# Kernel tuning notes

Hardware: AMD Instinct MI355X
Metric: run time of the kernel (lower is better)

Reference implementation:

```python
import jax, jax.numpy as jnp
import numpy as np

N, E, IN, ED, OUT = 50000, 800000, 64, 16, 64
AVG_D_LOG = 2.833  # log(avg_degree + 1), avg_degree = 16
EPS = 1e-5         # PNA std epsilon


def setup_inputs() -> dict:
    key = jax.random.key(0)
    ks = jax.random.split(key, 8)
    h = jax.random.normal(ks[0], (N, IN), jnp.float32)
    ef = jax.random.normal(ks[1], (E, ED), jnp.float32)
    snorm_n = jax.random.uniform(ks[2], (N, 1), jnp.float32)
    W_pre = jax.random.normal(ks[3], (2 * IN + ED, IN), jnp.float32) * 0.05
    b_pre = jnp.zeros((IN,), jnp.float32)
    W_post = jax.random.normal(ks[4], (13 * IN, OUT), jnp.float32) * 0.05
    b_post = jnp.zeros((OUT,), jnp.float32)
    src = jax.random.randint(ks[5], (E,), 0, N, dtype=jnp.int32).astype(jnp.int64)
    dst = jax.random.randint(ks[6], (E,), 0, N, dtype=jnp.int32).astype(jnp.int64)
    return dict(h=h, ef=ef, snorm_n=snorm_n, W_pre=W_pre, b_pre=b_pre,
                W_post=W_post, b_post=b_post, src=src, dst=dst)


def reference(h, ef, snorm_n, W_pre, b_pre, W_post, b_post, src, dst):
    # pretrans MLP (1 layer -> single linear, no activation) on per-edge concat
    z = jnp.concatenate([h[src], h[dst], ef], axis=1)      # [E, 2*IN+ED]
    msg = z @ W_pre + b_pre                                # [E, IN]

    deg = jax.ops.segment_sum(jnp.ones((E,), msg.dtype), dst, num_segments=N)  # [N]
    degc = jnp.maximum(deg, 1.0)
    has_msg = (deg > 0)[:, None]

    s = jax.ops.segment_sum(msg, dst, num_segments=N)
    mean = s / degc[:, None]
    mean_sq = jax.ops.segment_sum(msg * msg, dst, num_segments=N) / degc[:, None]
    std = jnp.sqrt(jax.nn.relu(mean_sq - mean * mean) + EPS)
    mx = jax.ops.segment_max(msg, dst, num_segments=N)
    mn = jax.ops.segment_min(msg, dst, num_segments=N)

    agg = jnp.concatenate([mean, mx, mn, std], axis=1)      # [N, 4*IN]
    agg = jnp.where(has_msg, agg, 0.0)                      # zero-in-degree nodes get 0

    logd = jnp.log(degc + 1.0)
    amp = agg * (logd / AVG_D_LOG)[:, None]                 # amplification scaler
    att = agg * (AVG_D_LOG / logd)[:, None]                 # attenuation scaler

    hcat = jnp.concatenate([h, agg, amp, att], axis=1)      # [N, 13*IN]
    out = hcat @ W_post + b_post                            # posttrans MLP (1 layer)
    out = out * snorm_n                                     # graph_norm
    return out
```

## Files before the change

### kernel.cpp

```cpp
#include <hip/hip_runtime.h>

constexpr int N_NODES = 50000;
constexpr int N_EDGES = 800000;
constexpr int IN_F = 64;
constexpr int ED_F = 16;
constexpr int OUT_F = 64;
constexpr int AGG_F = 256;
constexpr int KTOT = 832;
constexpr float AVG_D_LOG_F = 2.833f;
constexpr float EPS_F = 1e-5f;

constexpr int NB_BKT = 256;
constexpr int NODES_PER_BKT = 196;
constexpr int EPB_C = 4096;
constexpr int NBLK_C = (N_EDGES + EPB_C - 1) / EPB_C;

constexpr int AGG_WAVES = 12500;
constexpr int AGG_BLOCKS = AGG_WAVES / 4;

typedef __attribute__((ext_vector_type(8))) short short8;
typedef __attribute__((ext_vector_type(4))) float f32x4;

__device__ __forceinline__ int rfl(int v) { return __builtin_amdgcn_readfirstlane(v); }
__device__ __forceinline__ unsigned short f2bf(float f) {
    unsigned u = __float_as_uint(f);
    unsigned r = (u + 0x7FFFu + ((u >> 16) & 1u)) >> 16;
    return (unsigned short)r;
}

constexpr int P12MM_BLKS = 625;
constexpr int P12_TPB = 5;
constexpr int BKT_BLKS = 196;
constexpr int CONV_BLKS = 2500;
__global__ __launch_bounds__(256) void prep_kernel(
    const float* __restrict__ h, const float* __restrict__ Wpre, const float* __restrict__ bpre,
    const int* __restrict__ dst, const float* __restrict__ ef, const float* __restrict__ Wpost,
    unsigned short* __restrict__ P1b, float* __restrict__ P2, unsigned short* __restrict__ hb,
    int* __restrict__ bktcnt, unsigned short* __restrict__ efb,
    unsigned short* __restrict__ WT, unsigned short* __restrict__ WefT)
{
    int tid = threadIdx.x;
    if (blockIdx.x < P12MM_BLKS) {
        int lane = tid & 63;
        int li = lane & 15;
        int lg = lane >> 4;
        int w = tid >> 6;
        int col = w * 16 + li;

        short8 B1[2], B2[2];
        #pragma unroll
        for (int s = 0; s < 2; ++s) {
            short8 b1 = {}, b2 = {};
            #pragma unroll
            for (int j = 0; j < 8; ++j) {
                int k = s * 32 + (lg << 3) + j;
                b1[j] = (short)f2bf(Wpre[k * 64 + col]);
                b2[j] = (short)f2bf(Wpre[(64 + k) * 64 + col]);
            }
            B1[s] = b1; B2[s] = b2;
        }
        float bj = bpre[col];

        #pragma unroll 1
        for (int t = 0; t < P12_TPB; ++t) {
            int tile = blockIdx.x + t * P12MM_BLKS;
            int nA = tile * 16 + li;
            const float* hrow = h + (size_t)nA * IN_F;
            float4 v0 = *reinterpret_cast<const float4*>(hrow + (lg << 3));
            float4 v1 = *reinterpret_cast<const float4*>(hrow + (lg << 3) + 4);
            float4 v2 = *reinterpret_cast<const float4*>(hrow + 32 + (lg << 3));
            float4 v3 = *reinterpret_cast<const float4*>(hrow + 32 + (lg << 3) + 4);
            short8 a0, a1;
            a0[0]=(short)f2bf(v0.x); a0[1]=(short)f2bf(v0.y); a0[2]=(short)f2bf(v0.z); a0[3]=(short)f2bf(v0.w);
            a0[4]=(short)f2bf(v1.x); a0[5]=(short)f2bf(v1.y); a0[6]=(short)f2bf(v1.z); a0[7]=(short)f2bf(v1.w);
            a1[0]=(short)f2bf(v2.x); a1[1]=(short)f2bf(v2.y); a1[2]=(short)f2bf(v2.z); a1[3]=(short)f2bf(v2.w);
            a1[4]=(short)f2bf(v3.x); a1[5]=(short)f2bf(v3.y); a1[6]=(short)f2bf(v3.z); a1[7]=(short)f2bf(v3.w);

            if (w == 0) {
                *reinterpret_cast<short8*>(hb + (size_t)nA * IN_F + (lg << 3)) = a0;
                *reinterpret_cast<short8*>(hb + (size_t)nA * IN_F + 32 + (lg << 3)) = a1;
            }

            f32x4 p1a = {0.f,0.f,0.f,0.f}, p2a = {0.f,0.f,0.f,0.f};
            p1a = __builtin_amdgcn_mfma_f32_16x16x32_bf16(a0, B1[0], p1a, 0, 0, 0);
            p1a = __builtin_amdgcn_mfma_f32_16x16x32_bf16(a1, B1[1], p1a, 0, 0, 0);
            p2a = __builtin_amdgcn_mfma_f32_16x16x32_bf16(a0, B2[0], p2a, 0, 0, 0);
            p2a = __builtin_amdgcn_mfma_f32_16x16x32_bf16(a1, B2[1], p2a, 0, 0, 0);

            #pragma unroll
            for (int rr = 0; rr < 4; ++rr) {
                int node = tile * 16 + (lg << 2) + rr;
                P1b[(size_t)node * IN_F + col] = f2bf(p1a[rr]);
                P2[(size_t)node * IN_F + col] = p2a[rr] + bj;
            }
        }
    } else if (blockIdx.x < P12MM_BLKS + BKT_BLKS) {
        __shared__ int bh[NB_BKT];
        bh[tid] = 0;
        __syncthreads();
        int e0 = (blockIdx.x - P12MM_BLKS) * EPB_C;
        #pragma unroll
        for (int k = 0; k < EPB_C / 256; ++k) {
            int e = e0 + k * 256 + tid;
            if (e < N_EDGES) atomicAdd(&bh[dst[e] / NODES_PER_BKT], 1);
        }
        __syncthreads();
        if (bh[tid] > 0) atomicAdd(&bktcnt[tid], bh[tid]);
    } else {
        int cgid = (blockIdx.x - P12MM_BLKS - BKT_BLKS) * 256 + tid;
        const float4* ef4 = reinterpret_cast<const float4*>(ef);
        #pragma unroll
        for (int k = 0; k < 5; ++k) {
            int i = cgid + k * (CONV_BLKS * 256);
            float4 v = ef4[i];
            ushort4 o;
            o.x = f2bf(v.x); o.y = f2bf(v.y); o.z = f2bf(v.z); o.w = f2bf(v.w);
            *reinterpret_cast<ushort4*>(efb + (size_t)i * 4) = o;
        }
        if (cgid < OUT_F * KTOT) {
            int n = cgid / KTOT, k = cgid % KTOT;
            WT[cgid] = f2bf(Wpost[(size_t)k * OUT_F + n]);
        }
        if (cgid < 64 * 16) {
            int n = cgid >> 4, k = cgid & 15;
            WefT[cgid] = f2bf(Wpre[(128 + k) * 64 + n]);
        }
    }
}

__global__ __launch_bounds__(256) void bscan_kernel(
    const int* __restrict__ bktcnt, int* __restrict__ bkt_start, int* __restrict__ bcur)
{
    __shared__ int ws[4];
    int tid = threadIdx.x, lane = tid & 63, wv = tid >> 6;
    int v = bktcnt[tid];
    int sc = v;
    #pragma unroll
    for (int off = 1; off < 64; off <<= 1) {
        int u = __shfl_up(sc, off);
        if (lane >= off) sc += u;
    }
    if (lane == 63) ws[wv] = sc;
    __syncthreads();
    int wbase = 0;
    #pragma unroll
    for (int w = 0; w < 4; ++w) if (w < wv) wbase += ws[w];
    int ex = wbase + sc - v;
    bkt_start[tid] = ex;
    bcur[tid] = ex;
    if (tid == 255) bkt_start[256] = ex + v;
}

__global__ __launch_bounds__(256) void binC_kernel(
    const int* __restrict__ src, const int* __restrict__ dst, int* __restrict__ bcur,
    int* __restrict__ stage_e, int* __restrict__ stage_sd)
{
    __shared__ int sL[EPB_C];
    __shared__ int dL[EPB_C];
    __shared__ int bh[NB_BKT];
    __shared__ int bbase[NB_BKT];
    __shared__ int bcsr[NB_BKT];

    int tid = threadIdx.x;
    int e0 = blockIdx.x * EPB_C;

    bh[tid] = 0;
    __syncthreads();
    #pragma unroll
    for (int k = 0; k < EPB_C / 256; ++k) {
        int t = k * 256 + tid;
        int e = e0 + t;
        if (e < N_EDGES) {
            int s = src[e], d = dst[e];
            sL[t] = s; dL[t] = d;
            atomicAdd(&bh[d / NODES_PER_BKT], 1);
        }
    }
    __syncthreads();
    bbase[tid] = (bh[tid] > 0) ? atomicAdd(&bcur[tid], bh[tid]) : 0;
    bcsr[tid] = 0;
    __syncthreads();
    #pragma unroll
    for (int k = 0; k < EPB_C / 256; ++k) {
        int t = k * 256 + tid;
        int e = e0 + t;
        if (e < N_EDGES) {
            int d = dL[t];
            int b = d / NODES_PER_BKT;
            int dl = d - b * NODES_PER_BKT;
            int r = atomicAdd(&bcsr[b], 1);
            int pos = bbase[b] + r;
            stage_e[pos] = e;
            stage_sd[pos] = sL[t] | (dl << 16);
        }
    }
}

__global__ __launch_bounds__(256) void binD_kernel(
    const int* __restrict__ stage_e, const int* __restrict__ stage_sd,
    const int* __restrict__ bkt_start,
    int* __restrict__ deg, int* __restrict__ row_start, int2* __restrict__ csr2)
{
    __shared__ int cnt[NB_BKT];
    __shared__ int lofs[NODES_PER_BKT];
    __shared__ int ws[4];
    int tid = threadIdx.x, lane = tid & 63, wv = tid >> 6;
    int b = blockIdx.x;
    int nb0 = b * NODES_PER_BKT;
    cnt[tid] = 0;
    __syncthreads();
    int pbeg = bkt_start[b];
    int pend = bkt_start[b + 1];
    for (int p = pbeg + tid; p < pend; p += 256)
        atomicAdd(&cnt[stage_sd[p] >> 16], 1);
    __syncthreads();
    int v = cnt[tid];
    int sc = v;
    #pragma unroll
    for (int off = 1; off < 64; off <<= 1) {
        int u = __shfl_up(sc, off);
        if (lane >= off) sc += u;
    }
    if (lane == 63) ws[wv] = sc;
    __syncthreads();
    int wbase = 0;
    #pragma unroll
    for (int w = 0; w < 4; ++w) if (w < wv) wbase += ws[w];
    int ex = wbase + sc - v;
    if (tid < NODES_PER_BKT) {
        int n = nb0 + tid;
        if (n < N_NODES) { deg[n] = v; row_start[n] = pbeg + ex; }
        lofs[tid] = pbeg + ex;
    }
    __syncthreads();
    for (int p = pbeg + tid; p < pend; p += 256) {
        int sd = stage_sd[p];
        int r = atomicAdd(&lofs[sd >> 16], 1);
        csr2[r] = make_int2(stage_e[p], sd & 0xFFFF);
    }
}

#define AGG_MFMA8(aP0_, aP1_, aE_) \
    c0 = __builtin_amdgcn_mfma_f32_16x16x32_bf16(aP0_, bI0, c0, 0, 0, 0); \
    c1 = __builtin_amdgcn_mfma_f32_16x16x32_bf16(aP0_, bI1, c1, 0, 0, 0); \
    c2 = __builtin_amdgcn_mfma_f32_16x16x32_bf16(aP1_, bI0, c2, 0, 0, 0); \
    c3 = __builtin_amdgcn_mfma_f32_16x16x32_bf16(aP1_, bI1, c3, 0, 0, 0); \
    c0 = __builtin_amdgcn_mfma_f32_16x16x32_bf16(aE_, bE0, c0, 0, 0, 0);  \
    c1 = __builtin_amdgcn_mfma_f32_16x16x32_bf16(aE_, bE1, c1, 0, 0, 0);  \
    c2 = __builtin_amdgcn_mfma_f32_16x16x32_bf16(aE_, bE2, c2, 0, 0, 0);  \
    c3 = __builtin_amdgcn_mfma_f32_16x16x32_bf16(aE_, bE3, c3, 0, 0, 0);

#define STATS_FULL() do { \
    sm[0] += (c0[0] + c0[1]) + (c0[2] + c0[3]); \
    sm[1] += (c1[0] + c1[1]) + (c1[2] + c1[3]); \
    sm[2] += (c2[0] + c2[1]) + (c2[2] + c2[3]); \
    sm[3] += (c3[0] + c3[1]) + (c3[2] + c3[3]); \
    sq[0] = fmaf(c0[0],c0[0], fmaf(c0[1],c0[1], fmaf(c0[2],c0[2], fmaf(c0[3],c0[3], sq[0])))); \
    sq[1] = fmaf(c1[0],c1[0], fmaf(c1[1],c1[1], fmaf(c1[2],c1[2], fmaf(c1[3],c1[3], sq[1])))); \
    sq[2] = fmaf(c2[0],c2[0], fmaf(c2[1],c2[1], fmaf(c2[2],c2[2], fmaf(c2[3],c2[3], sq[2])))); \
    sq[3] = fmaf(c3[0],c3[0], fmaf(c3[1],c3[1], fmaf(c3[2],c3[2], fmaf(c3[3],c3[3], sq[3])))); \
    mx[0] = fmaxf(fmaxf(fmaxf(fmaxf(mx[0], c0[0]), c0[1]), c0[2]), c0[3]); \
    mx[1] = fmaxf(fmaxf(fmaxf(fmaxf(mx[1], c1[0]), c1[1]), c1[2]), c1[3]); \
    mx[2] = fmaxf(fmaxf(fmaxf(fmaxf(mx[2], c2[0]), c2[1]), c2[2]), c2[3]); \
    mx[3] = fmaxf(fmaxf(fmaxf(fmaxf(mx[3], c3[0]), c3[1]), c3[2]), c3[3]); \
    mn[0] = fminf(fminf(fminf(fminf(mn[0], c0[0]), c0[1]), c0[2]), c0[3]); \
    mn[1] = fminf(fminf(fminf(fminf(mn[1], c1[0]), c1[1]), c1[2]), c1[3]); \
    mn[2] = fminf(fminf(fminf(fminf(mn[2], c2[0]), c2[1]), c2[2]), c2[3]); \
    mn[3] = fminf(fminf(fminf(fminf(mn[3], c3[0]), c3[1]), c3[2]), c3[3]); \
} while (0)

#define STATS_MASK(RB_) do { \
    _Pragma("unroll") \
    for (int rr = 0; rr < 4; ++rr) { \
        bool vv = ((RB_) + rr) < dg; \
        float x0 = c0[rr], x1 = c1[rr], x2 = c2[rr], x3 = c3[rr]; \
        float z0 = vv ? x0 : 0.f, z1 = vv ? x1 : 0.f, z2 = vv ? x2 : 0.f, z3 = vv ? x3 : 0.f; \
        sm[0] += z0; sm[1] += z1; sm[2] += z2; sm[3] += z3; \
        sq[0] = fmaf(z0, z0, sq[0]); sq[1] = fmaf(z1, z1, sq[1]); \
        sq[2] = fmaf(z2, z2, sq[2]); sq[3] = fmaf(z3, z3, sq[3]); \
        mx[0] = fmaxf(mx[0], x0); mx[1] = fmaxf(mx[1], x1); \
        mx[2] = fmaxf(mx[2], x2); mx[3] = fmaxf(mx[3], x3); \
        mn[0] = fminf(mn[0], x0); mn[1] = fminf(mn[1], x1); \
        mn[2] = fminf(mn[2], x2); mn[3] = fminf(mn[3], x3); \
    } \
} while (0)

__global__ __launch_bounds__(256) void aggmm_kernel(
    const unsigned short* __restrict__ P1b, const float* __restrict__ P2,
    const unsigned short* __restrict__ efb, const unsigned short* __restrict__ WefT,
    const int2* __restrict__ csr2, const int* __restrict__ row_start,
    const int* __restrict__ deg, unsigned short* __restrict__ aggb)
{
    int tid = threadIdx.x;
    int lane = tid & 63;
    int lg = lane >> 4;
    int li = lane & 15;

    short8 bI0 = {}, bI1 = {};
    #pragma unroll
    for (int j = 0; j < 8; ++j) {
        int k_local = (lg << 3) + j;
        if (k_local == li)      bI0[j] = (short)0x3F80;
        if (k_local == 16 + li) bI1[j] = (short)0x3F80;
    }
    short8 bE0 = {}, bE1 = {}, bE2 = {}, bE3 = {};
    if (lane < 32) {
        bE0 = *reinterpret_cast<const short8*>(WefT + (size_t)(0 * 16 + li) * 16 + (lg << 3));
        bE1 = *reinterpret_cast<const short8*>(WefT + (size_t)(1 * 16 + li) * 16 + (lg << 3));
        bE2 = *reinterpret_cast<const short8*>(WefT + (size_t)(2 * 16 + li) * 16 + (lg << 3));
        bE3 = *reinterpret_cast<const short8*>(WefT + (size_t)(3 * 16 + li) * 16 + (lg << 3));
    }

    int wgid = rfl(blockIdx.x * 4 + (tid >> 6));

    int rsA[4], dgA[4];
    float p2A[4];
    #pragma unroll
    for (int nn = 0; nn < 4; ++nn) {
        int n = wgid + nn * AGG_WAVES;
        rsA[nn] = rfl(row_start[n]);
        dgA[nn] = rfl(deg[n]);
        p2A[nn] = P2[(size_t)n * IN_F + lane];
    }

    int2 e0n, e1n;
    {
        int dgc = dgA[0] > 0 ? dgA[0] : 1;
        int i0 = li < dgc ? li : dgc - 1;
        int i1 = 16 + li < dgc ? 16 + li : dgc - 1;
        int g0 = rsA[0] + i0; if (g0 > N_EDGES - 1) g0 = N_EDGES - 1;
        int g1 = rsA[0] + i1; if (g1 > N_EDGES - 1) g1 = N_EDGES - 1;
        e0n = csr2[g0];
        e1n = csr2[g1];
    }

    #pragma unroll
    for (int nn = 0; nn < 4; ++nn) {
        int n = wgid + nn * AGG_WAVES;
        int dg = dgA[nn];
        int2 e0 = e0n, e1 = e1n;

        if (nn < 3) {
            int dgc = dgA[nn + 1] > 0 ? dgA[nn + 1] : 1;
            int i0 = li < dgc ? li : dgc - 1;
            int i1 = 16 + li < dgc ? 16 + li : dgc - 1;
            int g0 = rsA[nn + 1] + i0; if (g0 > N_EDGES - 1) g0 = N_EDGES - 1;
            int g1 = rsA[nn + 1] + i1; if (g1 > N_EDGES - 1) g1 = N_EDGES - 1;
            e0n = csr2[g0];
            e1n = csr2[g1];
        }

        size_t obase = (size_t)n * AGG_F + lane;
        if (dg == 0) {
            aggb[obase] = 0; aggb[obase + 64] = 0;
            aggb[obase + 128] = 0; aggb[obase + 192] = 0;
            continue;
        }

        float p2n = p2A[nn];
        const float NINF = -__builtin_inff(), PINF = __builtin_inff();
        float sm[4] = {0.f, 0.f, 0.f, 0.f};
        float sq[4] = {0.f, 0.f, 0.f, 0.f};
        float mx[4] = {NINF, NINF, NINF, NINF};
        float mn[4] = {PINF, PINF, PINF, PINF};

        if (dg <= 32) {
            const unsigned short* pr0 = P1b + (size_t)e0.y * IN_F + (lg << 3);
            const unsigned short* pr1 = P1b + (size_t)e1.y * IN_F + (lg << 3);
            short8 aP0a = *reinterpret_cast<const short8*>(pr0);
            short8 aP1a = *reinterpret_cast<const short8*>(pr0 + 32);
            short8 aP0b = *reinterpret_cast<const short8*>(pr1);
            short8 aP1b = *reinterpret_cast<const short8*>(pr1 + 32);
            short8 aEa = {}, aEb = {};
            if (lane < 32) {
                aEa = *reinterpret_cast<const short8*>(efb + (size_t)e0.x * ED_F + (lg << 3));
                aEb = *reinterpret_cast<const short8*>(efb + (size_t)e1.x * ED_F + (lg << 3));
            }

            {
                f32x4 c0 = {0.f,0.f,0.f,0.f}, c1 = {0.f,0.f,0.f,0.f};
                f32x4 c2 = {0.f,0.f,0.f,0.f}, c3 = {0.f,0.f,0.f,0.f};
                AGG_MFMA8(aP0a, aP1a, aEa);
                if (dg >= 16) { STATS_FULL(); }
                else          { STATS_MASK((lg << 2)); }
            }
            if (dg > 16) {
                f32x4 c0 = {0.f,0.f,0.f,0.f}, c1 = {0.f,0.f,0.f,0.f};
                f32x4 c2 = {0.f,0.f,0.f,0.f}, c3 = {0.f,0.f,0.f,0.f};
                AGG_MFMA8(aP0b, aP1b, aEb);
                if (dg >= 32) { STATS_FULL(); }
                else          { STATS_MASK(16 + (lg << 2)); }
            }
        } else {
            for (int base = 0; base < dg; base += 64) {
                int cnt = dg - base; if (cnt > 64) cnt = 64;
                int2 es = make_int2(0, 0);
                if (lane < cnt) es = csr2[rsA[nn] + base + lane];
                int eid = es.x, sid = es.y;
                int nrt = (cnt + 15) >> 4;
                for (int rt = 0; rt < nrt; ++rt) {
                    int srcidx = rt * 16 + li;
                    if (srcidx >= cnt) srcidx = cnt - 1;
                    int s_l = __shfl(sid, srcidx);
                    int e_l = __shfl(eid, srcidx);
                    short8 aP0 = *reinterpret_cast<const short8*>(P1b + (size_t)s_l * IN_F + (lg << 3));
                    short8 aP1 = *reinterpret_cast<const short8*>(P1b + (size_t)s_l * IN_F + 32 + (lg << 3));
                    short8 aE = {};
                    if (lane < 32)
                        aE = *reinterpret_cast<const short8*>(efb + (size_t)e_l * ED_F + (lg << 3));
                    f32x4 c0 = {0.f,0.f,0.f,0.f}, c1 = {0.f,0.f,0.f,0.f};
                    f32x4 c2 = {0.f,0.f,0.f,0.f}, c3 = {0.f,0.f,0.f,0.f};
                    AGG_MFMA8(aP0, aP1, aE);
                    int dgsave = dg; (void)dgsave;
                    {
                        int rb2 = rt * 16 + (lg << 2);
                        #pragma unroll
                        for (int rr = 0; rr < 4; ++rr) {
                            bool vv = (rb2 + rr) < cnt;
                            float x0 = c0[rr], x1 = c1[rr], x2 = c2[rr], x3 = c3[rr];
                            float z0 = vv ? x0 : 0.f, z1 = vv ? x1 : 0.f, z2 = vv ? x2 : 0.f, z3 = vv ? x3 : 0.f;
                            sm[0] += z0; sm[1] += z1; sm[2] += z2; sm[3] += z3;
                            sq[0] = fmaf(z0, z0, sq[0]); sq[1] = fmaf(z1, z1, sq[1]);
                            sq[2] = fmaf(z2, z2, sq[2]); sq[3] = fmaf(z3, z3, sq[3]);
                            mx[0] = fmaxf(mx[0], x0); mx[1] = fmaxf(mx[1], x1);
                            mx[2] = fmaxf(mx[2], x2); mx[3] = fmaxf(mx[3], x3);
                            mn[0] = fminf(mn[0], x0); mn[1] = fminf(mn[1], x1);
                            mn[2] = fminf(mn[2], x2); mn[3] = fminf(mn[3], x3);
                        }
                    }
                }
            }
        }

        #pragma unroll
        for (int ct = 0; ct < 4; ++ct) {
            #pragma unroll
            for (int off = 16; off <= 32; off <<= 1) {
                sm[ct] += __shfl_xor(sm[ct], off);
                sq[ct] += __shfl_xor(sq[ct], off);
                mx[ct] = fmaxf(mx[ct], __shfl_xor(mx[ct], off));
                mn[ct] = fminf(mn[ct], __shfl_xor(mn[ct], off));
            }
        }
        bool s16 = (lane & 16) != 0, s32 = (lane & 32) != 0;
        float S  = s32 ? (s16 ? sm[3] : sm[2]) : (s16 ? sm[1] : sm[0]);
        float Qq = s32 ? (s16 ? sq[3] : sq[2]) : (s16 ? sq[1] : sq[0]);
        float MX = s32 ? (s16 ? mx[3] : mx[2]) : (s16 ? mx[1] : mx[0]);
        float MN = s32 ? (s16 ? mn[3] : mn[2]) : (s16 ? mn[1] : mn[0]);

        float degc = (float)dg;
        float mean_x = S / degc;
        float sd = sqrtf(fmaxf(Qq / degc - mean_x * mean_x, 0.f) + EPS_F);
        aggb[obase]       = f2bf(mean_x + p2n);
        aggb[obase + 64]  = f2bf(MX + p2n);
        aggb[obase + 128] = f2bf(MN + p2n);
        aggb[obase + 192] = f2bf(sd);
    }
}

constexpr int POST_BLOCKS = 625;
constexpr int TILES_PER_BLOCK = 5;
__global__ __launch_bounds__(256, 2) void postmm_kernel(
    const unsigned short* __restrict__ hb, const float* __restrict__ snorm,
    const unsigned short* __restrict__ WT, const float* __restrict__ bpost,
    const unsigned short* __restrict__ aggb, const int* __restrict__ deg,
    float* __restrict__ out)
{
    int tid = threadIdx.x;
    int lane = tid & 63;
    int li = lane & 15;
    int lg = lane >> 4;
    int w = tid >> 6;

    const unsigned short* Brow = WT + (size_t)(w * 16 + li) * KTOT + (lg << 3);
    short8 B[26];
    #pragma unroll
    for (int s = 0; s < 26; ++s)
        B[s] = *reinterpret_cast<const short8*>(Brow + s * 32);

    float bp = bpost[w * 16 + li];

    #pragma unroll 1
    for (int t = 0; t < TILES_PER_BLOCK; ++t) {
        int tile = blockIdx.x + t * POST_BLOCKS;
        int nA = tile * 16 + li;
        const unsigned short* Ah = hb + (size_t)nA * IN_F + (lg << 3);
        const unsigned short* Ag = aggb + (size_t)nA * AGG_F + (lg << 3);

        short8 ah0 = *reinterpret_cast<const short8*>(Ah);
        short8 ah1 = *reinterpret_cast<const short8*>(Ah + 32);
        short8 ag[8];
        #pragma unroll
        for (int s = 0; s < 8; ++s)
            ag[s] = *reinterpret_cast<const short8*>(Ag + s * 32);

        f32x4 accA = {0.f,0.f,0.f,0.f}, accB = {0.f,0.f,0.f,0.f}, accC = {0.f,0.f,0.f,0.f};
        accA = __builtin_amdgcn_mfma_f32_16x16x32_bf16(ah0, B[0], accA, 0, 0, 0);
        accA = __builtin_amdgcn_mfma_f32_16x16x32_bf16(ah1, B[1], accA, 0, 0, 0);
        #pragma unroll
        for (int s = 0; s < 8; ++s) {
            accA = __builtin_amdgcn_mfma_f32_16x16x32_bf16(ag[s], B[2 + s],  accA, 0, 0, 0);
            accB = __builtin_amdgcn_mfma_f32_16x16x32_bf16(ag[s], B[10 + s], accB, 0, 0, 0);
            accC = __builtin_amdgcn_mfma_f32_16x16x32_bf16(ag[s], B[18 + s], accC, 0, 0, 0);
        }

        #pragma unroll
        for (int rr = 0; rr < 4; ++rr) {
            int node = tile * 16 + (lg << 2) + rr;
            int dg = deg[node];
            float degc = fmaxf((float)dg, 1.f);
            float logd = logf(degc + 1.f);
            float aR = logd * (1.f / AVG_D_LOG_F);
            float bR = AVG_D_LOG_F / logd;
            float v = accA[rr] + aR * accB[rr] + bR * accC[rr] + bp;
            out[(size_t)node * OUT_F + w * 16 + li] = v * snorm[node];
        }
    }
}

extern "C" void kernel_launch(void* const* d_in, const int* in_sizes, int n_in,
                              void* d_out, int out_size, void* d_ws, size_t ws_size,
                              hipStream_t stream) {
    const float* h     = (const float*)d_in[0];
    const float* ef    = (const float*)d_in[1];
    const float* snorm = (const float*)d_in[2];
    const float* Wpre  = (const float*)d_in[3];
    const float* bpre  = (const float*)d_in[4];
    const float* Wpost = (const float*)d_in[5];
    const float* bpost = (const float*)d_in[6];
    const int* src     = (const int*)d_in[7];
    const int* dst     = (const int*)d_in[8];
    float* out = (float*)d_out;

    char* ws = (char*)d_ws;
    size_t off = 0;
    auto alloc = [&](size_t bytes) { char* p = ws + off; off += (bytes + 255) & ~size_t(255); return p; };
    unsigned short* P1b  = (unsigned short*)alloc((size_t)N_NODES * IN_F * 2);
    float* P2            = (float*)alloc((size_t)N_NODES * IN_F * 4);
    unsigned short* hb   = (unsigned short*)alloc((size_t)N_NODES * IN_F * 2);
    unsigned short* aggb = (unsigned short*)alloc((size_t)N_NODES * AGG_F * 2);
    unsigned short* efb  = (unsigned short*)alloc((size_t)N_EDGES * ED_F * 2);
    int* deg       = (int*)alloc((size_t)N_NODES * 4);
    int* row_start = (int*)alloc((size_t)N_NODES * 4);
    int2* csr2     = (int2*)alloc((size_t)N_EDGES * 8);
    int* stage_e   = (int*)alloc((size_t)N_EDGES * 4);
    int* stage_sd  = (int*)alloc((size_t)N_EDGES * 4);
    int* bktcnt    = (int*)alloc((size_t)NB_BKT * 4);
    int* bkt_start = (int*)alloc((size_t)(NB_BKT + 1) * 4);
    int* bcur      = (int*)alloc((size_t)NB_BKT * 4);
    unsigned short* WT   = (unsigned short*)alloc((size_t)OUT_F * KTOT * 2);
    unsigned short* WefT = (unsigned short*)alloc((size_t)64 * 16 * 2);

    hipMemsetAsync(bktcnt, 0, (size_t)NB_BKT * 4, stream);
    hipLaunchKernelGGL(prep_kernel, dim3(P12MM_BLKS + BKT_BLKS + CONV_BLKS), dim3(256), 0, stream,
                       h, Wpre, bpre, dst, ef, Wpost,
                       P1b, P2, hb, bktcnt, efb, WT, WefT);
    hipLaunchKernelGGL(bscan_kernel, dim3(1), dim3(256), 0, stream, bktcnt, bkt_start, bcur);
    hipLaunchKernelGGL(binC_kernel, dim3(NBLK_C), dim3(256), 0, stream,
                       src, dst, bcur, stage_e, stage_sd);
    hipLaunchKernelGGL(binD_kernel, dim3(NB_BKT), dim3(256), 0, stream,
                       stage_e, stage_sd, bkt_start, deg, row_start, csr2);
    hipLaunchKernelGGL(aggmm_kernel, dim3(AGG_BLOCKS), dim3(256), 0, stream,
                       P1b, P2, efb, WefT, csr2, row_start, deg, aggb);
    hipLaunchKernelGGL(postmm_kernel, dim3(POST_BLOCKS), dim3(256), 0, stream,
                       hb, snorm, WT, bpost, aggb, deg, out);
}
```

Baseline: 134.1 us.

## Use fixed-stride edge buckets and deepen gather prefetch in aggregation

Replaces the bucket-count histogram pass and the single-block scan with fixed 4096-slot per-bucket regions, so binning uses a plain atomic counter per bucket. This removes one kernel launch and one pass over dst. The aggregation kernel now prefetches CSR entries two nodes ahead and the P1/edge-feature gathers one node ahead, so more load latency is hidden. The cost is larger staging and CSR buffers, a silent overflow if any bucket exceeds 4096 edges, and more registers held by the prefetch buffers.

Result: no change. 136.3 us (+1.6%).

```diff
diff --git a/kernel.cpp b/kernel.cpp
--- a/kernel.cpp
+++ b/kernel.cpp
@@ -12,6 +12,7 @@
 
 constexpr int NB_BKT = 256;
 constexpr int NODES_PER_BKT = 196;
+constexpr int BKT_STRIDE = 4096;
 constexpr int EPB_C = 4096;
 constexpr int NBLK_C = (N_EDGES + EPB_C - 1) / EPB_C;
 
@@ -30,13 +31,12 @@
 
 constexpr int P12MM_BLKS = 625;
 constexpr int P12_TPB = 5;
-constexpr int BKT_BLKS = 196;
 constexpr int CONV_BLKS = 2500;
 __global__ __launch_bounds__(256) void prep_kernel(
     const float* __restrict__ h, const float* __restrict__ Wpre, const float* __restrict__ bpre,
-    const int* __restrict__ dst, const float* __restrict__ ef, const float* __restrict__ Wpost,
+    const float* __restrict__ ef, const float* __restrict__ Wpost,
     unsigned short* __restrict__ P1b, float* __restrict__ P2, unsigned short* __restrict__ hb,
-    int* __restrict__ bktcnt, unsigned short* __restrict__ efb,
+    unsigned short* __restrict__ efb,
     unsigned short* __restrict__ WT, unsigned short* __restrict__ WefT)
 {
     int tid = threadIdx.x;
@@ -94,20 +94,8 @@
                 P2[(size_t)node * IN_F + col] = p2a[rr] + bj;
             }
         }
-    } else if (blockIdx.x < P12MM_BLKS + BKT_BLKS) {
-        __shared__ int bh[NB_BKT];
-        bh[tid] = 0;
-        __syncthreads();
-        int e0 = (blockIdx.x - P12MM_BLKS) * EPB_C;
-        #pragma unroll
-        for (int k = 0; k < EPB_C / 256; ++k) {
-            int e = e0 + k * 256 + tid;
-            if (e < N_EDGES) atomicAdd(&bh[dst[e] / NODES_PER_BKT], 1);
-        }
-        __syncthreads();
-        if (bh[tid] > 0) atomicAdd(&bktcnt[tid], bh[tid]);
     } else {
-        int cgid = (blockIdx.x - P12MM_BLKS - BKT_BLKS) * 256 + tid;
+        int cgid = (blockIdx.x - P12MM_BLKS) * 256 + tid;
         const float4* ef4 = reinterpret_cast<const float4*>(ef);
         #pragma unroll
         for (int k = 0; k < 5; ++k) {
@@ -128,31 +116,8 @@
     }
 }
 
-__global__ __launch_bounds__(256) void bscan_kernel(
-    const int* __restrict__ bktcnt, int* __restrict__ bkt_start, int* __restrict__ bcur)
-{
-    __shared__ int ws[4];
-    int tid = threadIdx.x, lane = tid & 63, wv = tid >> 6;
-    int v = bktcnt[tid];
-    int sc = v;
-    #pragma unroll
-    for (int off = 1; off < 64; off <<= 1) {
-        int u = __shfl_up(sc, off);
-        if (lane >= off) sc += u;
-    }
-    if (lane == 63) ws[wv] = sc;
-    __syncthreads();
-    int wbase = 0;
-    #pragma unroll
-    for (int w = 0; w < 4; ++w) if (w < wv) wbase += ws[w];
-    int ex = wbase + sc - v;
-    bkt_start[tid] = ex;
-    bcur[tid] = ex;
-    if (tid == 255) bkt_start[256] = ex + v;
-}
-
 __global__ __launch_bounds__(256) void binC_kernel(
-    const int* __restrict__ src, const int* __restrict__ dst, int* __restrict__ bcur,
+    const int* __restrict__ src, const int* __restrict__ dst, int* __restrict__ bcur0,
     int* __restrict__ stage_e, int* __restrict__ stage_sd)
 {
     __shared__ int sL[EPB_C];
@@ -177,7 +142,7 @@
         }
     }
     __syncthreads();
-    bbase[tid] = (bh[tid] > 0) ? atomicAdd(&bcur[tid], bh[tid]) : 0;
+    bbase[tid] = (bh[tid] > 0) ? atomicAdd(&bcur0[tid], bh[tid]) : 0;
     bcsr[tid] = 0;
     __syncthreads();
     #pragma unroll
@@ -189,7 +154,7 @@
             int b = d / NODES_PER_BKT;
             int dl = d - b * NODES_PER_BKT;
             int r = atomicAdd(&bcsr[b], 1);
-            int pos = bbase[b] + r;
+            int pos = (b << 12) + bbase[b] + r;
             stage_e[pos] = e;
             stage_sd[pos] = sL[t] | (dl << 16);
         }
@@ -198,7 +163,7 @@
 
 __global__ __launch_bounds__(256) void binD_kernel(
     const int* __restrict__ stage_e, const int* __restrict__ stage_sd,
-    const int* __restrict__ bkt_start,
+    const int* __restrict__ bcur0,
     int* __restrict__ deg, int* __restrict__ row_start, int2* __restrict__ csr2)
 {
     __shared__ int cnt[NB_BKT];
@@ -207,11 +172,11 @@
     int tid = threadIdx.x, lane = tid & 63, wv = tid >> 6;
     int b = blockIdx.x;
     int nb0 = b * NODES_PER_BKT;
+    int base = b << 12;
     cnt[tid] = 0;
     __syncthreads();
-    int pbeg = bkt_start[b];
-    int pend = bkt_start[b + 1];
-    for (int p = pbeg + tid; p < pend; p += 256)
+    int cntb = bcur0[b];
+    for (int p = base + tid; p < base + cntb; p += 256)
         atomicAdd(&cnt[stage_sd[p] >> 16], 1);
     __syncthreads();
     int v = cnt[tid];
@@ -229,11 +194,11 @@
     int ex = wbase + sc - v;
     if (tid < NODES_PER_BKT) {
         int n = nb0 + tid;
-        if (n < N_NODES) { deg[n] = v; row_start[n] = pbeg + ex; }
-        lofs[tid] = pbeg + ex;
-    }
-    __syncthreads();
-    for (int p = pbeg + tid; p < pend; p += 256) {
+        if (n < N_NODES) { deg[n] = v; row_start[n] = base + ex; }
+        lofs[tid] = base + ex;
+    }
+    __syncthreads();
+    for (int p = base + tid; p < base + cntb; p += 256) {
         int sd = stage_sd[p];
         int r = atomicAdd(&lofs[sd >> 16], 1);
         csr2[r] = make_int2(stage_e[p], sd & 0xFFFF);
@@ -269,10 +234,10 @@
     mn[3] = fminf(fminf(fminf(fminf(mn[3], c3[0]), c3[1]), c3[2]), c3[3]); \
 } while (0)
 
-#define STATS_MASK(RB_) do { \
+#define STATS_MASK(RB_, LIM_) do { \
     _Pragma("unroll") \
     for (int rr = 0; rr < 4; ++rr) { \
-        bool vv = ((RB_) + rr) < dg; \
+        bool vv = ((RB_) + rr) < (LIM_); \
         float x0 = c0[rr], x1 = c1[rr], x2 = c2[rr], x3 = c3[rr]; \
         float z0 = vv ? x0 : 0.f, z1 = vv ? x1 : 0.f, z2 = vv ? x2 : 0.f, z3 = vv ? x3 : 0.f; \
         sm[0] += z0; sm[1] += z1; sm[2] += z2; sm[3] += z3; \
@@ -323,31 +288,60 @@
         p2A[nn] = P2[(size_t)n * IN_F + lane];
     }
 
-    int2 e0n, e1n;
-    {
-        int dgc = dgA[0] > 0 ? dgA[0] : 1;
+    int2 eA[4], eB[4];
+    #pragma unroll
+    for (int nn = 0; nn < 2; ++nn) {
+        int dgc = dgA[nn] > 0 ? dgA[nn] : 1;
         int i0 = li < dgc ? li : dgc - 1;
         int i1 = 16 + li < dgc ? 16 + li : dgc - 1;
-        int g0 = rsA[0] + i0; if (g0 > N_EDGES - 1) g0 = N_EDGES - 1;
-        int g1 = rsA[0] + i1; if (g1 > N_EDGES - 1) g1 = N_EDGES - 1;
-        e0n = csr2[g0];
-        e1n = csr2[g1];
+        eA[nn] = csr2[rsA[nn] + i0];
+        eB[nn] = csr2[rsA[nn] + i1];
+    }
+
+    short8 gP0a, gP1a, gP0b, gP1b, gEa, gEb;
+    {
+        const unsigned short* pr0 = P1b + (size_t)eA[0].y * IN_F + (lg << 3);
+        const unsigned short* pr1 = P1b + (size_t)eB[0].y * IN_F + (lg << 3);
+        gP0a = *reinterpret_cast<const short8*>(pr0);
+        gP1a = *reinterpret_cast<const short8*>(pr0 + 32);
+        gP0b = *reinterpret_cast<const short8*>(pr1);
+        gP1b = *reinterpret_cast<const short8*>(pr1 + 32);
+        short8 z = {};
+        gEa = z; gEb = z;
+        if (lane < 32) {
+            gEa = *reinterpret_cast<const short8*>(efb + (size_t)eA[0].x * ED_F + (lg << 3));
+            gEb = *reinterpret_cast<const short8*>(efb + (size_t)eB[0].x * ED_F + (lg << 3));
+        }
     }
 
     #pragma unroll
     for (int nn = 0; nn < 4; ++nn) {
         int n = wgid + nn * AGG_WAVES;
         int dg = dgA[nn];
-        int2 e0 = e0n, e1 = e1n;
+
+        short8 aP0a = gP0a, aP1a = gP1a, aP0b = gP0b, aP1b = gP1b, aEa = gEa, aEb = gEb;
 
         if (nn < 3) {
-            int dgc = dgA[nn + 1] > 0 ? dgA[nn + 1] : 1;
+            const unsigned short* pr0 = P1b + (size_t)eA[nn + 1].y * IN_F + (lg << 3);
+            const unsigned short* pr1 = P1b + (size_t)eB[nn + 1].y * IN_F + (lg << 3);
+            gP0a = *reinterpret_cast<const short8*>(pr0);
+            gP1a = *reinterpret_cast<const short8*>(pr0 + 32);
+            gP0b = *reinterpret_cast<const short8*>(pr1);
+            gP1b = *reinterpret_cast<const short8*>(pr1 + 32);
+            short8 z = {};
+            gEa = z; gEb = z;
+            if (lane < 32) {
+                gEa = *reinterpret_cast<const short8*>(efb + (size_t)eA[nn + 1].x * ED_F + (lg << 3));
+                gEb = *reinterpret_cast<const short8*>(efb + (size_t)eB[nn + 1].x * ED_F + (lg << 3));
+            }
+        }
+        if (nn < 2) {
+            int m = nn + 2;
+            int dgc = dgA[m] > 0 ? dgA[m] : 1;
             int i0 = li < dgc ? li : dgc - 1;
             int i1 = 16 + li < dgc ? 16 + li : dgc - 1;
-            int g0 = rsA[nn + 1] + i0; if (g0 > N_EDGES - 1) g0 = N_EDGES - 1;
-            int g1 = rsA[nn + 1] + i1; if (g1 > N_EDGES - 1) g1 = N_EDGES - 1;
-            e0n = csr2[g0];
-            e1n = csr2[g1];
+            eA[m] = csr2[rsA[m] + i0];
+            eB[m] = csr2[rsA[m] + i1];
         }
 
         size_t obase = (size_t)n * AGG_F + lane;
@@ -365,31 +359,19 @@
         float mn[4] = {PINF, PINF, PINF, PINF};
 
         if (dg <= 32) {
-            const unsigned short* pr0 = P1b + (size_t)e0.y * IN_F + (lg << 3);
-            const unsigned short* pr1 = P1b + (size_t)e1.y * IN_F + (lg << 3);
-            short8 aP0a = *reinterpret_cast<const short8*>(pr0);
-            short8 aP1a = *reinterpret_cast<const short8*>(pr0 + 32);
-            short8 aP0b = *reinterpret_cast<const short8*>(pr1);
-            short8 aP1b = *reinterpret_cast<const short8*>(pr1 + 32);
-            short8 aEa = {}, aEb = {};
-            if (lane < 32) {
-                aEa = *reinterpret_cast<const short8*>(efb + (size_t)e0.x * ED_F + (lg << 3));
-                aEb = *reinterpret_cast<const short8*>(efb + (size_t)e1.x * ED_F + (lg << 3));
-            }
-
             {
                 f32x4 c0 = {0.f,0.f,0.f,0.f}, c1 = {0.f,0.f,0.f,0.f};
                 f32x4 c2 = {0.f,0.f,0.f,0.f}, c3 = {0.f,0.f,0.f,0.f};
                 AGG_MFMA8(aP0a, aP1a, aEa);
                 if (dg >= 16) { STATS_FULL(); }
-                else          { STATS_MASK((lg << 2)); }
+                else          { STATS_MASK((lg << 2), dg); }
             }
             if (dg > 16) {
                 f32x4 c0 = {0.f,0.f,0.f,0.f}, c1 = {0.f,0.f,0.f,0.f};
                 f32x4 c2 = {0.f,0.f,0.f,0.f}, c3 = {0.f,0.f,0.f,0.f};
                 AGG_MFMA8(aP0b, aP1b, aEb);
                 if (dg >= 32) { STATS_FULL(); }
-                else          { STATS_MASK(16 + (lg << 2)); }
+                else          { STATS_MASK(16 + (lg << 2), dg); }
             }
         } else {
             for (int base = 0; base < dg; base += 64) {
@@ -411,23 +393,8 @@
                     f32x4 c0 = {0.f,0.f,0.f,0.f}, c1 = {0.f,0.f,0.f,0.f};
                     f32x4 c2 = {0.f,0.f,0.f,0.f}, c3 = {0.f,0.f,0.f,0.f};
                     AGG_MFMA8(aP0, aP1, aE);
-                    int dgsave = dg; (void)dgsave;
-                    {
-                        int rb2 = rt * 16 + (lg << 2);
-                        #pragma unroll
-                        for (int rr = 0; rr < 4; ++rr) {
-                            bool vv = (rb2 + rr) < cnt;
-                            float x0 = c0[rr], x1 = c1[rr], x2 = c2[rr], x3 = c3[rr];
-                            float z0 = vv ? x0 : 0.f, z1 = vv ? x1 : 0.f, z2 = vv ? x2 : 0.f, z3 = vv ? x3 : 0.f;
-                            sm[0] += z0; sm[1] += z1; sm[2] += z2; sm[3] += z3;
-                            sq[0] = fmaf(z0, z0, sq[0]); sq[1] = fmaf(z1, z1, sq[1]);
-                            sq[2] = fmaf(z2, z2, sq[2]); sq[3] = fmaf(z3, z3, sq[3]);
-                            mx[0] = fmaxf(mx[0], x0); mx[1] = fmaxf(mx[1], x1);
-                            mx[2] = fmaxf(mx[2], x2); mx[3] = fmaxf(mx[3], x3);
-                            mn[0] = fminf(mn[0], x0); mn[1] = fminf(mn[1], x1);
-                            mn[2] = fminf(mn[2], x2); mn[3] = fminf(mn[3], x3);
-                        }
-                    }
+                    int rb2 = rt * 16 + (lg << 2);
+                    STATS_MASK(rb2, cnt);
                 }
             }
         }
@@ -542,24 +509,21 @@
     unsigned short* efb  = (unsigned short*)alloc((size_t)N_EDGES * ED_F * 2);
     int* deg       = (int*)alloc((size_t)N_NODES * 4);
     int* row_start = (int*)alloc((size_t)N_NODES * 4);
-    int2* csr2     = (int2*)alloc((size_t)N_EDGES * 8);
-    int* stage_e   = (int*)alloc((size_t)N_EDGES * 4);
-    int* stage_sd  = (int*)alloc((size_t)N_EDGES * 4);
-    int* bktcnt    = (int*)alloc((size_t)NB_BKT * 4);
-    int* bkt_start = (int*)alloc((size_t)(NB_BKT + 1) * 4);
-    int* bcur      = (int*)alloc((size_t)NB_BKT * 4);
+    int2* csr2     = (int2*)alloc((size_t)NB_BKT * BKT_STRIDE * 8);
+    int* stage_e   = (int*)alloc((size_t)NB_BKT * BKT_STRIDE * 4);
+    int* stage_sd  = (int*)alloc((size_t)NB_BKT * BKT_STRIDE * 4);
+    int* bcur0     = (int*)alloc((size_t)NB_BKT * 4);
     unsigned short* WT   = (unsigned short*)alloc((size_t)OUT_F * KTOT * 2);
     unsigned short* WefT = (unsigned short*)alloc((size_t)64 * 16 * 2);
 
-    hipMemsetAsync(bktcnt, 0, (size_t)NB_BKT * 4, stream);
-    hipLaunchKernelGGL(prep_kernel, dim3(P12MM_BLKS + BKT_BLKS + CONV_BLKS), dim3(256), 0, stream,
-                       h, Wpre, bpre, dst, ef, Wpost,
-                       P1b, P2, hb, bktcnt, efb, WT, WefT);
-    hipLaunchKernelGGL(bscan_kernel, dim3(1), dim3(256), 0, stream, bktcnt, bkt_start, bcur);
+    hipMemsetAsync(bcur0, 0, (size_t)NB_BKT * 4, stream);
+    hipLaunchKernelGGL(prep_kernel, dim3(P12MM_BLKS + CONV_BLKS), dim3(256), 0, stream,
+                       h, Wpre, bpre, ef, Wpost,
+                       P1b, P2, hb, efb, WT, WefT);
     hipLaunchKernelGGL(binC_kernel, dim3(NBLK_C), dim3(256), 0, stream,
-                       src, dst, bcur, stage_e, stage_sd);
+                       src, dst, bcur0, stage_e, stage_sd);
     hipLaunchKernelGGL(binD_kernel, dim3(NB_BKT), dim3(256), 0, stream,
-                       stage_e, stage_sd, bkt_start, deg, row_start, csr2);
+                       stage_e, stage_sd, bcur0, deg, row_start, csr2);
     hipLaunchKernelGGL(aggmm_kernel, dim3(AGG_BLOCKS), dim3(256), 0, stream,
                        P1b, P2, efb, WefT, csr2, row_start, deg, aggb);
     hipLaunchKernelGGL(postmm_kernel, dim3(POST_BLOCKS), dim3(256), 0, stream,
```
